# Kernel optimization log

Hardware: AMD Instinct MI355X
Metric: run time of the kernel (lower is better)

## Reference

```python
import jax, jax.numpy as jnp
import numpy as np

B = 131072
H = 128          # hidden_dim
U = H // 2       # uniform_dim = 64
NH = 4           # num_heads
HD = U // NH     # head_dim = 16
OUT = 128        # output_dim
EPS = 1e-5


def setup_inputs() -> dict:
    key = jax.random.key(0)
    ks = jax.random.split(key, 32)
    s = 0.05
    d = {}
    d["x"] = jax.random.normal(ks[0], (B, 58), dtype=jnp.float32)
    # component encoders (Linear -> ReLU -> Dropout(eval))
    d["W_phys"] = jax.random.normal(ks[1], (H // 2, 29)) * s
    d["b_phys"] = jax.random.normal(ks[2], (H // 2,)) * s
    d["W_obj"] = jax.random.normal(ks[3], (H // 4, 15)) * s
    d["b_obj"] = jax.random.normal(ks[4], (H // 4,)) * s
    d["W_mine"] = jax.random.normal(ks[5], (H // 8, 8)) * s
    d["b_mine"] = jax.random.normal(ks[6], (H // 8,)) * s
    d["W_prog"] = jax.random.normal(ks[7], (H // 8, 3)) * s
    d["b_prog"] = jax.random.normal(ks[8], (H // 8,)) * s
    d["W_seq"] = jax.random.normal(ks[9], (H // 8, 3)) * s
    d["b_seq"] = jax.random.normal(ks[10], (H // 8,)) * s
    # projections to uniform_dim
    d["P_phys"] = jax.random.normal(ks[11], (U, H // 2)) * s
    d["pb_phys"] = jax.random.normal(ks[12], (U,)) * s
    d["P_obj"] = jax.random.normal(ks[13], (U, H // 4)) * s
    d["pb_obj"] = jax.random.normal(ks[14], (U,)) * s
    d["P_mine"] = jax.random.normal(ks[15], (U, H // 8)) * s
    d["pb_mine"] = jax.random.normal(ks[16], (U,)) * s
    d["P_prog"] = jax.random.normal(ks[17], (U, H // 8)) * s
    d["pb_prog"] = jax.random.normal(ks[18], (U,)) * s
    d["P_seq"] = jax.random.normal(ks[19], (U, H // 8)) * s
    d["pb_seq"] = jax.random.normal(ks[20], (U,)) * s
    # multi-head attention (torch packed in_proj + out_proj)
    d["Wqkv"] = jax.random.normal(ks[21], (3 * U, U)) * s
    d["bqkv"] = jax.random.normal(ks[22], (3 * U,)) * s
    d["Wo"] = jax.random.normal(ks[23], (U, U)) * s
    d["bo"] = jax.random.normal(ks[24], (U,)) * s
    # layernorm + pool projection
    d["gamma"] = jnp.ones((U,), dtype=jnp.float32)
    d["beta"] = jnp.zeros((U,), dtype=jnp.float32)
    d["Wp"] = jax.random.normal(ks[25], (OUT, U)) * s
    d["bp"] = jax.random.normal(ks[26], (OUT,)) * s
    return d


def _forward(x, W_phys, b_phys, W_obj, b_obj, W_mine, b_mine, W_prog, b_prog,
             W_seq, b_seq, P_phys, pb_phys, P_obj, pb_obj, P_mine, pb_mine,
             P_prog, pb_prog, P_seq, pb_seq, Wqkv, bqkv, Wo, bo,
             gamma, beta, Wp, bp):
    # split 58-dim state into semantic components
    phys, obj, mine = x[:, :29], x[:, 29:44], x[:, 44:52]
    prog, seq = x[:, 52:55], x[:, 55:58]
    relu = jax.nn.relu
    # component encoders (dropout is identity in eval)
    phys_f = relu(phys @ W_phys.T + b_phys)
    obj_f = relu(obj @ W_obj.T + b_obj)
    mine_f = relu(mine @ W_mine.T + b_mine)
    prog_f = relu(prog @ W_prog.T + b_prog)
    seq_f = relu(seq @ W_seq.T + b_seq)
    # project each component to uniform_dim token
    tokens = jnp.stack([
        phys_f @ P_phys.T + pb_phys,
        obj_f @ P_obj.T + pb_obj,
        mine_f @ P_mine.T + pb_mine,
        prog_f @ P_prog.T + pb_prog,
        seq_f @ P_seq.T + pb_seq,
    ], axis=1)  # [B, 5, U]
    # multi-head self-attention (batch_first, torch semantics)
    qkv = tokens @ Wqkv.T + bqkv                      # [B, 5, 3U]
    q, k, v = jnp.split(qkv, 3, axis=-1)
    Bn, S, _ = tokens.shape
    q = q.reshape(Bn, S, NH, HD)
    k = k.reshape(Bn, S, NH, HD)
    v = v.reshape(Bn, S, NH, HD)
    scores = jnp.einsum('bqhd,bkhd->bhqk', q, k) / np.sqrt(HD).astype(np.float32)
    attn = jax.nn.softmax(scores, axis=-1)
    ctx = jnp.einsum('bhqk,bkhd->bqhd', attn, v).reshape(Bn, S, U)
    attn_out = ctx @ Wo.T + bo
    # residual + layernorm
    h = tokens + attn_out
    mu = h.mean(axis=-1, keepdims=True)
    var = ((h - mu) ** 2).mean(axis=-1, keepdims=True)
    h = (h - mu) * jax.lax.rsqrt(var + EPS) * gamma + beta
    # mean pool over the 5 tokens, project, relu (output dropout = identity)
    pooled = h.mean(axis=1)
    return relu(pooled @ Wp.T + bp)  # [B, OUT]


def reference(x, W_phys, b_phys, W_obj, b_obj, W_mine, b_mine, W_prog, b_prog,
              W_seq, b_seq, P_phys, pb_phys, P_obj, pb_obj, P_mine, pb_mine,
              P_prog, pb_prog, P_seq, pb_seq, Wqkv, bqkv, Wo, bo,
              gamma, beta, Wp, bp):
    return _forward(x, W_phys, b_phys, W_obj, b_obj, W_mine, b_mine, W_prog,
                    b_prog, W_seq, b_seq, P_phys, pb_phys, P_obj, pb_obj,
                    P_mine, pb_mine, P_prog, pb_prog, P_seq, pb_seq,
                    Wqkv, bqkv, Wo, bo, gamma, beta, Wp, bp)
```

## Files before the change

kernel.cpp:

```cpp
#include <hip/hip_runtime.h>


#define B_TOTAL 131072
#define NBLK    (B_TOTAL / 64)

typedef _Float16 f16;
typedef __attribute__((ext_vector_type(2))) _Float16 f16x2;
typedef __attribute__((ext_vector_type(8))) _Float16 f16x8;
typedef __attribute__((ext_vector_type(8))) __fp16   mfma8;
typedef __attribute__((ext_vector_type(4))) float    f32x4;

#define W_EW    0
#define W_TOKW  4608
#define W_QKVW  10752
#define W_WOW   29184
#define W_WPW   33280
#define W_ENCB  37376
#define W_TOKB  37520
#define W_QKVB  37840
#define W_BPB   38800
#define W_TOTAL 38928

__device__ __forceinline__ unsigned pk_rne(float a, float b) {
    f16x2 r; r.x = (_Float16)a; r.y = (_Float16)b;
    return __builtin_bit_cast(unsigned, r);
}

extern "C" __global__ void k_prep(
    const float* __restrict__ Wph, const float* __restrict__ bph,
    const float* __restrict__ Wob, const float* __restrict__ bob,
    const float* __restrict__ Wmi, const float* __restrict__ bmi,
    const float* __restrict__ Wpr, const float* __restrict__ bpr,
    const float* __restrict__ Wse, const float* __restrict__ bse,
    const float* __restrict__ Pph, const float* __restrict__ pbph,
    const float* __restrict__ Pob, const float* __restrict__ pbob,
    const float* __restrict__ Pmi, const float* __restrict__ pbmi,
    const float* __restrict__ Ppr, const float* __restrict__ pbpr,
    const float* __restrict__ Pse, const float* __restrict__ pbse,
    const float* __restrict__ Wqkv, const float* __restrict__ bqkv,
    const float* __restrict__ Wo,  const float* __restrict__ bo,
    const float* __restrict__ Wp,  const float* __restrict__ bp,
    unsigned* __restrict__ ws)
{
    int idx = blockIdx.x * 256 + threadIdx.x;
    if (idx >= W_TOTAL) return;
    float* wsf = (float*)ws;

    if (idx < W_TOKW) {
        int w2 = idx, blk = w2 >> 8, r = w2 & 255, lane = r >> 2, pr = r & 3;
        int nt = blk >> 1, ks = blk & 1;
        int n = nt * 16 + (lane & 15);
        float v[2];
#pragma unroll
        for (int e = 0; e < 2; e++) {
            int k = ks * 32 + ((lane >> 4) << 3) + pr * 2 + e;
            float val = 0.f;
            if (n < 64)       { if (k < 29) val = Wph[n*29 + k]; }
            else if (n < 96)  { int kk = k - 29; if (kk >= 0 && kk < 15) val = Wob[(n-64)*15 + kk]; }
            else if (n < 112) { int kk = k - 44; if (kk >= 0 && kk < 8)  val = Wmi[(n-96)*8  + kk]; }
            else if (n < 128) { int kk = k - 52; if (kk >= 0 && kk < 3)  val = Wpr[(n-112)*3 + kk]; }
            else              { int kk = k - 55; if (kk >= 0 && kk < 3)  val = Wse[(n-128)*3 + kk]; }
            v[e] = val;
        }
        ws[idx] = pk_rne(v[0], v[1]);
    } else if (idx < W_QKVW) {
        int w2 = idx - W_TOKW, blk = w2 >> 8, r = w2 & 255, lane = r >> 2, pr = r & 3;
        int t, nt, ks;
        if (blk < 8) { t = 0; nt = blk >> 1; ks = blk & 1; }
        else         { t = 1 + ((blk - 8) >> 2); nt = (blk - 8) & 3; ks = 0; }
        const float* P = (t==0)?Pph:(t==1)?Pob:(t==2)?Pmi:(t==3)?Ppr:Pse;
        int d = (t==0)?64:(t==1)?32:16;
        int n = nt * 16 + (lane & 15);
        float v[2];
#pragma unroll
        for (int e = 0; e < 2; e++) {
            int k = ks * 32 + ((lane >> 4) << 3) + pr * 2 + e;
            v[e] = (k < d) ? P[n*d + k] : 0.f;
        }
        ws[idx] = pk_rne(v[0], v[1]);
    } else if (idx < W_WOW) {
        int w2 = idx - W_QKVW, blk = w2 >> 8, r = w2 & 255, lane = r >> 2, pr = r & 3;
        int t, b2;
        if (blk < 24) { t = 0; b2 = blk; }
        else          { t = 1 + (blk - 24) / 12; b2 = (blk - 24) % 12; }
        int h, nt, ks;
        if (t == 0) { h = b2 / 6; int rem = b2 % 6; nt = rem >> 1; ks = rem & 1; }
        else        { h = b2 / 3; nt = b2 % 3; ks = 0; }
        const float* P = (t==0)?Pph:(t==1)?Pob:(t==2)?Pmi:(t==3)?Ppr:Pse;
        int d = (t==0)?64:(t==1)?32:16;
        int c = nt * 64 + h * 16 + (lane & 15);
        float v[2] = {0.f, 0.f};
#pragma unroll
        for (int e = 0; e < 2; e++) {
            int k = ks * 32 + ((lane >> 4) << 3) + pr * 2 + e;
            if (k < d) {
                float s = 0.f;
                for (int u = 0; u < 64; u++) s += Wqkv[c*64 + u] * P[u*d + k];
                v[e] = s;
            }
        }
        ws[idx] = pk_rne(v[0], v[1]);
    } else if (idx < W_WPW) {
        int w2 = idx - W_WOW, blk = w2 >> 8, r = w2 & 255, lane = r >> 2, pr = r & 3;
        int h = blk >> 2, nt = blk & 3;
        int n = nt * 16 + (lane & 15);
        float v[2];
#pragma unroll
        for (int e = 0; e < 2; e++) {
            int k = ((lane >> 4) << 3) + pr * 2 + e;
            v[e] = (k < 16) ? Wo[n*64 + h*16 + k] : 0.f;
        }
        ws[idx] = pk_rne(v[0], v[1]);
    } else if (idx < W_ENCB) {
        int w2 = idx - W_WPW, blk = w2 >> 8, r = w2 & 255, lane = r >> 2, pr = r & 3;
        int nt = blk >> 1, ks = blk & 1;
        int n = nt * 16 + (lane & 15);
        float v[2];
#pragma unroll
        for (int e = 0; e < 2; e++) {
            int k = ks * 32 + ((lane >> 4) << 3) + pr * 2 + e;
            v[e] = Wp[n*64 + k];
        }
        ws[idx] = pk_rne(v[0], v[1]);
    } else if (idx < W_TOKB) {
        int n = idx - W_ENCB;
        wsf[idx] = (n<64)?bph[n]:(n<96)?bob[n-64]:(n<112)?bmi[n-96]:(n<128)?bpr[n-112]:bse[n-128];
    } else if (idx < W_QKVB) {
        int r = idx - W_TOKB, t = r >> 6, u = r & 63;
        const float* pb = (t==0)?pbph:(t==1)?pbob:(t==2)?pbmi:(t==3)?pbpr:pbse;
        wsf[idx] = pb[u] + bo[u];
    } else if (idx < W_BPB) {
        int r = idx - W_QKVB, t = r / 192, c = r % 192;
        const float* pb = (t==0)?pbph:(t==1)?pbob:(t==2)?pbmi:(t==3)?pbpr:pbse;
        float s = bqkv[c];
        for (int u = 0; u < 64; u++) s += Wqkv[c*64 + u] * pb[u];
        wsf[idx] = s;
    } else {
        wsf[idx] = bp[idx - W_BPB];
    }
}

__device__ __forceinline__ f32x4 MFMA(f16x8 a, f16x8 b, f32x4 c) {
    return __builtin_amdgcn_mfma_f32_16x16x32_f16(
        __builtin_bit_cast(mfma8, a), __builtin_bit_cast(mfma8, b), c, 0, 0, 0);
}

__device__ __forceinline__ f16x8 ldB(const unsigned* __restrict__ W, int wordBase, int blk, int lane) {
    uint4 v = *((const uint4*)(W + wordBase) + (blk * 64 + lane));
    return __builtin_bit_cast(f16x8, v);
}

__device__ __forceinline__ f16x8 ldA(const f16* p, int stride, int row, int kbase, int lg) {
    return *(const f16x8*)(p + row * stride + kbase + lg * 8);
}

__device__ __forceinline__ void stC16(f16* base, int stride, int m0, int col0,
                                      f32x4 c, int l15, int lg) {
    int col = col0 + l15;
    int r0  = m0 + lg * 4;
#pragma unroll
    for (int r = 0; r < 4; r++) base[(r0 + r) * stride + col] = (f16)c[r];
}

extern "C" __global__ void __launch_bounds__(256, 2) k_main(
    const float* __restrict__ x,
    const float* __restrict__ gamma, const float* __restrict__ beta,
    const unsigned* __restrict__ W, float* __restrict__ out)
{
    __shared__ f16 f_lds[64 * 168];
    __shared__ __align__(16) char dyn_lds[41216];
    f16*      xb   = (f16*)dyn_lds;
    f16*      qkv  = (f16*)dyn_lds;
    unsigned* ctx  = (unsigned*)(dyn_lds + 30976);
    f16*      plA  = (f16*)dyn_lds;
    float*    outb = (float*)dyn_lds;

    const int tid  = threadIdx.x;
    const int lane = tid & 63;
    const int wv   = tid >> 6;
    const int l15  = lane & 15;
    const int lg   = lane >> 4;

    const float* wsf   = (const float*)W;
    const float* encb  = wsf + W_ENCB;
    const float* tokbp = wsf + W_TOKB;
    const float* qkvbp = wsf + W_QKVB;
    const float* bpp   = wsf + W_BPB;

    {
        unsigned* du = (unsigned*)dyn_lds;
        for (int i = tid; i < 2304; i += 256) du[i] = 0;
        unsigned* fu = (unsigned*)f_lds;
        for (int i = tid; i < 5376; i += 256) fu[i] = 0;
    }
    __syncthreads();
    {
        const float* xp = x + (size_t)blockIdx.x * (64 * 58);
        for (int i = tid; i < 3712; i += 256) {
            int s = i / 58, k = i - s * 58;
            xb[s * 72 + k] = (f16)xp[i];
        }
    }
    __syncthreads();

    {
        f32x4 accE[3][4];
#pragma unroll
        for (int i = 0; i < 3; i++) {
            int nt = wv + i * 4;
            if (nt < 9) {
                float be = encb[nt * 16 + l15];
#pragma unroll
                for (int mt = 0; mt < 4; mt++) accE[i][mt] = (f32x4){be, be, be, be};
            }
        }
#pragma unroll
        for (int ks = 0; ks < 2; ks++) {
            f16x8 a[4];
#pragma unroll
            for (int mt = 0; mt < 4; mt++) a[mt] = ldA(xb, 72, mt * 16 + l15, ks * 32, lg);
#pragma unroll
            for (int i = 0; i < 3; i++) {
                int nt = wv + i * 4;
                if (nt < 9) {
                    f16x8 b = ldB(W, W_EW, nt * 2 + ks, lane);
#pragma unroll
                    for (int mt = 0; mt < 4; mt++) accE[i][mt] = MFMA(a[mt], b, accE[i][mt]);
                }
            }
        }
#pragma unroll
        for (int i = 0; i < 3; i++) {
            int nt = wv + i * 4;
            if (nt < 9) {
#pragma unroll
                for (int mt = 0; mt < 4; mt++) {
                    f32x4 c = accE[i][mt];
#pragma unroll
                    for (int r = 0; r < 4; r++) c[r] = fmaxf(c[r], 0.f);
                    stC16(f_lds, 168, mt * 16, nt * 16, c, l15, lg);
                }
            }
        }
    }
    __syncthreads();

    f32x4 hf[5][4];

    {
#pragma unroll
        for (int t = 0; t < 5; t++)
#pragma unroll
            for (int nt = 0; nt < 4; nt++) {
                float bb = tokbp[t * 64 + nt * 16 + l15];
                hf[t][nt] = (f32x4){bb, bb, bb, bb};
            }
#pragma unroll
        for (int t = 0; t < 5; t++) {
            const int tokOff[5]  = {0, 64, 96, 112, 128};
            const int tokBase[5] = {0, 8, 12, 16, 20};
#pragma unroll
            for (int ks = 0; ks < 2; ks++) {
                if (ks == 0 || t == 0) {
                    f16x8 a = ldA(f_lds, 168, wv * 16 + l15, tokOff[t] + ks * 32, lg);
#pragma unroll
                    for (int nt = 0; nt < 4; nt++) {
                        int blk = (t == 0) ? (nt * 2 + ks) : (tokBase[t] + nt);
                        f16x8 b = ldB(W, W_TOKW, blk, lane);
                        hf[t][nt] = MFMA(a, b, hf[t][nt]);
                    }
                }
            }
        }
    }

    auto do_qkv = [&](int h) {
        const int tokOff[5]  = {0, 64, 96, 112, 128};
        const int qkvBase[5] = {0, 24, 36, 48, 60};
#pragma unroll
        for (int t = 0; t < 5; t++) {
            f32x4 aq[3];
#pragma unroll
            for (int nt = 0; nt < 3; nt++) {
                float bb = qkvbp[t * 192 + nt * 64 + h * 16 + l15];
                aq[nt] = (f32x4){bb, bb, bb, bb};
            }
#pragma unroll
            for (int ks = 0; ks < 2; ks++) {
                if (ks == 0 || t == 0) {
                    f16x8 a = ldA(f_lds, 168, wv * 16 + l15, tokOff[t] + ks * 32, lg);
#pragma unroll
                    for (int nt = 0; nt < 3; nt++) {
                        int blk = qkvBase[t] + ((t == 0) ? (h * 6 + nt * 2 + ks) : (h * 3 + nt));
                        f16x8 b = ldB(W, W_QKVW, blk, lane);
                        aq[nt] = MFMA(a, b, aq[nt]);
                    }
                }
            }
#pragma unroll
            for (int nt = 0; nt < 3; nt++)
                stC16(qkv, 242, wv * 16, t * 48 + nt * 16, aq[nt], l15, lg);
        }
    };

    auto do_att = [&]() {
        const int s    = tid & 63;
        const int role = wv;
        const f16x2* qr2 = (const f16x2*)(qkv + s * 242);
        float q0[16], q4[16];
#pragma unroll
        for (int d2 = 0; d2 < 8; d2++) {
            f16x2 p = qr2[role * 24 + d2];
            q0[2*d2] = (float)p.x; q0[2*d2+1] = (float)p.y;
        }
        if (role == 0) {
#pragma unroll
            for (int d2 = 0; d2 < 8; d2++) {
                f16x2 p = qr2[96 + d2];
                q4[2*d2] = (float)p.x; q4[2*d2+1] = (float)p.y;
            }
        }
        float p0[5], p4[5];
#pragma unroll
        for (int j = 0; j < 5; j++) {
            float a0 = 0.f, a4 = 0.f;
#pragma unroll
            for (int d2 = 0; d2 < 8; d2++) {
                f16x2 kp = qr2[j * 24 + 8 + d2];
                float k0 = (float)kp.x, k1 = (float)kp.y;
                a0 += q0[2*d2] * k0 + q0[2*d2+1] * k1;
                if (role == 0) a4 += q4[2*d2] * k0 + q4[2*d2+1] * k1;
            }
            p0[j] = a0 * 0.25f; p4[j] = a4 * 0.25f;
        }
        auto softmax5 = [](float* sc) {
            float m = fmaxf(fmaxf(fmaxf(sc[0], sc[1]), fmaxf(sc[2], sc[3])), sc[4]);
            float l = 0.f;
#pragma unroll
            for (int j = 0; j < 5; j++) { sc[j] = __expf(sc[j] - m); l += sc[j]; }
            float r = 1.f / l;
#pragma unroll
            for (int j = 0; j < 5; j++) sc[j] *= r;
        };
        softmax5(p0);
        if (role == 0) softmax5(p4);
        float c0[16], c4[16];
#pragma unroll
        for (int d = 0; d < 16; d++) { c0[d] = 0.f; c4[d] = 0.f; }
#pragma unroll
        for (int j = 0; j < 5; j++) {
#pragma unroll
            for (int d2 = 0; d2 < 8; d2++) {
                f16x2 vp = qr2[j * 24 + 16 + d2];
                float v0 = (float)vp.x, v1 = (float)vp.y;
                c0[2*d2]   += p0[j] * v0;
                c0[2*d2+1] += p0[j] * v1;
                if (role == 0) { c4[2*d2] += p4[j] * v0; c4[2*d2+1] += p4[j] * v1; }
            }
        }
        auto wrctx = [&](int i, const float* c) {
            int row = i * 64 + s;
            int vx  = ((row >> 2) & 3) << 1;
#pragma unroll
            for (int d2 = 0; d2 < 8; d2++)
                ctx[row * 8 + (d2 ^ vx)] = pk_rne(c[2*d2], c[2*d2+1]);
        };
        wrctx(role, c0);
        if (role == 0) wrctx(4, c4);
    };

    auto do_wo = [&](int h) {
        f16x8 bfr[4];
#pragma unroll
        for (int nt = 0; nt < 4; nt++) bfr[nt] = ldB(W, W_WOW, h * 4 + nt, lane);
#pragma unroll
        for (int t = 0; t < 5; t++) {
            int row = t * 64 + wv * 16 + l15;
            int vx  = ((row >> 2) & 3) << 1;
            uint2 a0 = *(const uint2*)&ctx[row * 8 + (((lg & 1) * 4 + 0) ^ vx)];
            uint2 a1 = *(const uint2*)&ctx[row * 8 + (((lg & 1) * 4 + 2) ^ vx)];
            if (lg >= 2) { a0.x = 0; a0.y = 0; a1.x = 0; a1.y = 0; }
            uint4 ua; ua.x = a0.x; ua.y = a0.y; ua.z = a1.x; ua.w = a1.y;
            f16x8 a = __builtin_bit_cast(f16x8, ua);
#pragma unroll
            for (int nt = 0; nt < 4; nt++) hf[t][nt] = MFMA(a, bfr[nt], hf[t][nt]);
        }
    };

    do_qkv(0);
    __syncthreads();
    for (int h = 0; h < 4; h++) {
        do_att();
        __syncthreads();
        do_wo(h);
        if (h < 3) do_qkv(h + 1);
        __syncthreads();
    }

    float g4[4], b4[4];
#pragma unroll
    for (int nt = 0; nt < 4; nt++) { g4[nt] = gamma[nt * 16 + l15]; b4[nt] = beta[nt * 16 + l15]; }
    f32x4 pool[4];
#pragma unroll
    for (int nt = 0; nt < 4; nt++) pool[nt] = (f32x4){0.f, 0.f, 0.f, 0.f};
#pragma unroll
    for (int t = 0; t < 5; t++) {
#pragma unroll
        for (int r = 0; r < 4; r++) {
            float sm = hf[t][0][r] + hf[t][1][r] + hf[t][2][r] + hf[t][3][r];
            sm += __shfl_xor(sm, 1); sm += __shfl_xor(sm, 2);
            sm += __shfl_xor(sm, 4); sm += __shfl_xor(sm, 8);
            float mu = sm * 0.015625f;
            float vs = 0.f;
#pragma unroll
            for (int nt = 0; nt < 4; nt++) { float d = hf[t][nt][r] - mu; vs += d * d; }
            vs += __shfl_xor(vs, 1); vs += __shfl_xor(vs, 2);
            vs += __shfl_xor(vs, 4); vs += __shfl_xor(vs, 8);
            float rs = rsqrtf(vs * 0.015625f + 1e-5f);
#pragma unroll
            for (int nt = 0; nt < 4; nt++)
                pool[nt][r] += (hf[t][nt][r] - mu) * rs * g4[nt] + b4[nt];
        }
    }
#pragma unroll
    for (int nt = 0; nt < 4; nt++) {
        f32x4 c = pool[nt];
#pragma unroll
        for (int r = 0; r < 4; r++) c[r] *= 0.2f;
        stC16(plA, 72, wv * 16, nt * 16, c, l15, lg);
    }
    __syncthreads();

    {
        f32x4 accP[8];
#pragma unroll
        for (int n2 = 0; n2 < 8; n2++) {
            float bb = bpp[n2 * 16 + l15];
            accP[n2] = (f32x4){bb, bb, bb, bb};
        }
#pragma unroll
        for (int ks = 0; ks < 2; ks++) {
            f16x8 a = ldA(plA, 72, wv * 16 + l15, ks * 32, lg);
#pragma unroll
            for (int n2 = 0; n2 < 8; n2++) {
                f16x8 b = ldB(W, W_WPW, n2 * 2 + ks, lane);
                accP[n2] = MFMA(a, b, accP[n2]);
            }
        }
        __syncthreads();
#pragma unroll
        for (int n2 = 0; n2 < 8; n2++) {
#pragma unroll
            for (int r = 0; r < 4; r++) {
                int srow = wv * 16 + lg * 4 + r;
                int col  = n2 * 16 + l15;
                outb[srow * 128 + (col ^ (((srow >> 2) & 3) << 4))] = fmaxf(accP[n2][r], 0.f);
            }
        }
    }
    __syncthreads();

    {
        float* og = out + (size_t)blockIdx.x * (64 * 128);
#pragma unroll
        for (int it = 0; it < 8; it++) {
            int i = tid + it * 256;
            int srow = i >> 5;
            int c4   = (i & 31) << 2;
            float4 v = *(const float4*)&outb[srow * 128 + (c4 ^ (((srow >> 2) & 3) << 4))];
            *(float4*)(og + srow * 128 + c4) = v;
        }
    }
}

extern "C" void kernel_launch(void* const* d_in, const int* in_sizes, int n_in,
                              void* d_out, int out_size, void* d_ws, size_t ws_size,
                              hipStream_t stream)
{
    const float* x      = (const float*)d_in[0];
    const float* W_phys = (const float*)d_in[1];
    const float* b_phys = (const float*)d_in[2];
    const float* W_obj  = (const float*)d_in[3];
    const float* b_obj  = (const float*)d_in[4];
    const float* W_mine = (const float*)d_in[5];
    const float* b_mine = (const float*)d_in[6];
    const float* W_prog = (const float*)d_in[7];
    const float* b_prog = (const float*)d_in[8];
    const float* W_seq  = (const float*)d_in[9];
    const float* b_seq  = (const float*)d_in[10];
    const float* P_phys = (const float*)d_in[11];
    const float* pb_phys= (const float*)d_in[12];
    const float* P_obj  = (const float*)d_in[13];
    const float* pb_obj = (const float*)d_in[14];
    const float* P_mine = (const float*)d_in[15];
    const float* pb_mine= (const float*)d_in[16];
    const float* P_prog = (const float*)d_in[17];
    const float* pb_prog= (const float*)d_in[18];
    const float* P_seq  = (const float*)d_in[19];
    const float* pb_seq = (const float*)d_in[20];
    const float* Wqkv   = (const float*)d_in[21];
    const float* bqkv   = (const float*)d_in[22];
    const float* Wo     = (const float*)d_in[23];
    const float* bo     = (const float*)d_in[24];
    const float* gamma  = (const float*)d_in[25];
    const float* beta   = (const float*)d_in[26];
    const float* Wp     = (const float*)d_in[27];
    const float* bp     = (const float*)d_in[28];

    unsigned* ws = (unsigned*)d_ws;

    k_prep<<<(W_TOTAL + 255) / 256, 256, 0, stream>>>(
        W_phys, b_phys, W_obj, b_obj, W_mine, b_mine, W_prog, b_prog, W_seq, b_seq,
        P_phys, pb_phys, P_obj, pb_obj, P_mine, pb_mine, P_prog, pb_prog, P_seq, pb_seq,
        Wqkv, bqkv, Wo, bo, Wp, bp, ws);

    k_main<<<NBLK, 256, 0, stream>>>(x, gamma, beta, ws, (float*)d_out);
}
```

Baseline: 283.6 us.

## Shrink LDS and restructure attention with swizzled layouts for three blocks per CU

Shrinks the shared scratch buffer so three blocks fit per CU (launch bounds raised from 2 to 3). The qkv buffer is re-laid out with XOR-swizzled row strides, and the attention is reworked to use packed f16 dot2 instructions with a split score/softmax phase and a separate context phase. The final output staging is done in two halves to fit the smaller buffer. This adds more barriers per head and raises register pressure under the tighter occupancy target, which risks spills.

```diff
diff --git a/kernel.cpp b/kernel.cpp
--- a/kernel.cpp
+++ b/kernel.cpp
@@ -24,6 +24,26 @@
 __device__ __forceinline__ unsigned pk_rne(float a, float b) {
     f16x2 r; r.x = (_Float16)a; r.y = (_Float16)b;
     return __builtin_bit_cast(unsigned, r);
+}
+
+__device__ __forceinline__ f16x2 u2h(unsigned u) { return __builtin_bit_cast(f16x2, u); }
+
+__device__ __forceinline__ float fdot2(f16x2 a, f16x2 b, float c) {
+#if __has_builtin(__builtin_amdgcn_fdot2)
+    typedef __fp16 hv2 __attribute__((ext_vector_type(2)));
+    return __builtin_amdgcn_fdot2(__builtin_bit_cast(hv2, a), __builtin_bit_cast(hv2, b), c, false);
+#else
+    return c + (float)a.x * (float)b.x + (float)a.y * (float)b.y;
+#endif
+}
+
+__device__ __forceinline__ float dot8(f16x8 a, f16x8 b, float c) {
+    uint4 ua = __builtin_bit_cast(uint4, a), ub = __builtin_bit_cast(uint4, b);
+    c = fdot2(u2h(ua.x), u2h(ub.x), c);
+    c = fdot2(u2h(ua.y), u2h(ub.y), c);
+    c = fdot2(u2h(ua.z), u2h(ub.z), c);
+    c = fdot2(u2h(ua.w), u2h(ub.w), c);
+    return c;
 }
 
 extern "C" __global__ void k_prep(
@@ -150,36 +170,30 @@
     return __builtin_bit_cast(f16x8, v);
 }
 
-__device__ __forceinline__ f16x8 ldA(const f16* p, int stride, int row, int kbase, int lg) {
-    return *(const f16x8*)(p + row * stride + kbase + lg * 8);
-}
-
-__device__ __forceinline__ void stC16(f16* base, int stride, int m0, int col0,
-                                      f32x4 c, int l15, int lg) {
-    int col = col0 + l15;
-    int r0  = m0 + lg * 4;
-#pragma unroll
-    for (int r = 0; r < 4; r++) base[(r0 + r) * stride + col] = (f16)c[r];
-}
-
-extern "C" __global__ void __launch_bounds__(256, 2) k_main(
+#define F_STRB  336
+#define Q_STRB  496
+
+__device__ __forceinline__ int fswz(int row, int colb) {
+    return (row * F_STRB + colb) ^ (((row >> 3) & 1) << 5);
+}
+__device__ __forceinline__ int qswz(int s, int bo) {
+    return (s * Q_STRB + bo) ^ (((s >> 3) & 1) << 5) ^ (((s >> 4) & 1) << 6);
+}
+
+extern "C" __global__ void __launch_bounds__(256, 3) k_main(
     const float* __restrict__ x,
     const float* __restrict__ gamma, const float* __restrict__ beta,
     const unsigned* __restrict__ W, float* __restrict__ out)
 {
-    __shared__ f16 f_lds[64 * 168];
-    __shared__ __align__(16) char dyn_lds[41216];
-    f16*      xb   = (f16*)dyn_lds;
-    f16*      qkv  = (f16*)dyn_lds;
-    unsigned* ctx  = (unsigned*)(dyn_lds + 30976);
-    f16*      plA  = (f16*)dyn_lds;
-    float*    outb = (float*)dyn_lds;
+    __shared__ __align__(16) f16  f_lds[64 * 168];
+    __shared__ __align__(16) char dyn[31744];
 
     const int tid  = threadIdx.x;
     const int lane = tid & 63;
     const int wv   = tid >> 6;
     const int l15  = lane & 15;
     const int lg   = lane >> 4;
+    const bool m4  = ((lane & 3) == wv);
 
     const float* wsf   = (const float*)W;
     const float* encb  = wsf + W_ENCB;
@@ -187,14 +201,34 @@
     const float* qkvbp = wsf + W_QKVB;
     const float* bpp   = wsf + W_BPB;
 
+    char* fb = (char*)f_lds;
+
+    auto ldA_f = [&](int row, int kf16) -> f16x8 {
+        return *(const f16x8*)(fb + fswz(row, kf16 * 2 + lg * 16));
+    };
+    auto stC_f = [&](int m0, int col0, f32x4 c) {
+#pragma unroll
+        for (int r = 0; r < 4; r++)
+            *(f16*)(fb + fswz(m0 + lg * 4 + r, (col0 + l15) * 2)) = (f16)c[r];
+    };
+    auto ldQ8 = [&](int s, int dw) -> f16x8 {
+        return *(const f16x8*)(dyn + qswz(s, dw * 4));
+    };
+    auto stC_qkv = [&](int m0, int col0, f32x4 c) {
+#pragma unroll
+        for (int r = 0; r < 4; r++)
+            *(f16*)(dyn + qswz(m0 + lg * 4 + r, (col0 + l15) * 2)) = (f16)c[r];
+    };
+
     {
-        unsigned* du = (unsigned*)dyn_lds;
-        for (int i = tid; i < 2304; i += 256) du[i] = 0;
         unsigned* fu = (unsigned*)f_lds;
         for (int i = tid; i < 5376; i += 256) fu[i] = 0;
+        unsigned* du = (unsigned*)dyn;
+        for (int i = tid; i < 2304; i += 256) du[i] = 0;
     }
     __syncthreads();
     {
+        f16* xb = (f16*)dyn;
         const float* xp = x + (size_t)blockIdx.x * (64 * 58);
         for (int i = tid; i < 3712; i += 256) {
             int s = i / 58, k = i - s * 58;
@@ -218,7 +252,10 @@
         for (int ks = 0; ks < 2; ks++) {
             f16x8 a[4];
 #pragma unroll
-            for (int mt = 0; mt < 4; mt++) a[mt] = ldA(xb, 72, mt * 16 + l15, ks * 32, lg);
+            for (int mt = 0; mt < 4; mt++) {
+                const char* p = dyn + (mt * 16 + l15) * 144 + ks * 64 + lg * 16;
+                a[mt] = *(const f16x8*)p;
+            }
 #pragma unroll
             for (int i = 0; i < 3; i++) {
                 int nt = wv + i * 4;
@@ -238,7 +275,7 @@
                     f32x4 c = accE[i][mt];
 #pragma unroll
                     for (int r = 0; r < 4; r++) c[r] = fmaxf(c[r], 0.f);
-                    stC16(f_lds, 168, mt * 16, nt * 16, c, l15, lg);
+                    stC_f(mt * 16, nt * 16, c);
                 }
             }
         }
@@ -246,8 +283,10 @@
     __syncthreads();
 
     f32x4 hf[5][4];
+    const int tokOff[5]  = {0, 64, 96, 112, 128};
 
     {
+        const int tokBase[5] = {0, 8, 12, 16, 20};
 #pragma unroll
         for (int t = 0; t < 5; t++)
 #pragma unroll
@@ -257,12 +296,10 @@
             }
 #pragma unroll
         for (int t = 0; t < 5; t++) {
-            const int tokOff[5]  = {0, 64, 96, 112, 128};
-            const int tokBase[5] = {0, 8, 12, 16, 20};
 #pragma unroll
             for (int ks = 0; ks < 2; ks++) {
                 if (ks == 0 || t == 0) {
-                    f16x8 a = ldA(f_lds, 168, wv * 16 + l15, tokOff[t] + ks * 32, lg);
+                    f16x8 a = ldA_f(wv * 16 + l15, tokOff[t] + ks * 32);
 #pragma unroll
                     for (int nt = 0; nt < 4; nt++) {
                         int blk = (t == 0) ? (nt * 2 + ks) : (tokBase[t] + nt);
@@ -275,7 +312,6 @@
     }
 
     auto do_qkv = [&](int h) {
-        const int tokOff[5]  = {0, 64, 96, 112, 128};
         const int qkvBase[5] = {0, 24, 36, 48, 60};
 #pragma unroll
         for (int t = 0; t < 5; t++) {
@@ -288,7 +324,7 @@
 #pragma unroll
             for (int ks = 0; ks < 2; ks++) {
                 if (ks == 0 || t == 0) {
-                    f16x8 a = ldA(f_lds, 168, wv * 16 + l15, tokOff[t] + ks * 32, lg);
+                    f16x8 a = ldA_f(wv * 16 + l15, tokOff[t] + ks * 32);
 #pragma unroll
                     for (int nt = 0; nt < 3; nt++) {
                         int blk = qkvBase[t] + ((t == 0) ? (h * 6 + nt * 2 + ks) : (h * 3 + nt));
@@ -299,86 +335,19 @@
             }
 #pragma unroll
             for (int nt = 0; nt < 3; nt++)
-                stC16(qkv, 242, wv * 16, t * 48 + nt * 16, aq[nt], l15, lg);
-        }
-    };
-
-    auto do_att = [&]() {
-        const int s    = tid & 63;
-        const int role = wv;
-        const f16x2* qr2 = (const f16x2*)(qkv + s * 242);
-        float q0[16], q4[16];
-#pragma unroll
-        for (int d2 = 0; d2 < 8; d2++) {
-            f16x2 p = qr2[role * 24 + d2];
-            q0[2*d2] = (float)p.x; q0[2*d2+1] = (float)p.y;
-        }
-        if (role == 0) {
-#pragma unroll
-            for (int d2 = 0; d2 < 8; d2++) {
-                f16x2 p = qr2[96 + d2];
-                q4[2*d2] = (float)p.x; q4[2*d2+1] = (float)p.y;
-            }
-        }
-        float p0[5], p4[5];
-#pragma unroll
-        for (int j = 0; j < 5; j++) {
-            float a0 = 0.f, a4 = 0.f;
-#pragma unroll
-            for (int d2 = 0; d2 < 8; d2++) {
-                f16x2 kp = qr2[j * 24 + 8 + d2];
-                float k0 = (float)kp.x, k1 = (float)kp.y;
-                a0 += q0[2*d2] * k0 + q0[2*d2+1] * k1;
-                if (role == 0) a4 += q4[2*d2] * k0 + q4[2*d2+1] * k1;
-            }
-            p0[j] = a0 * 0.25f; p4[j] = a4 * 0.25f;
-        }
-        auto softmax5 = [](float* sc) {
-            float m = fmaxf(fmaxf(fmaxf(sc[0], sc[1]), fmaxf(sc[2], sc[3])), sc[4]);
-            float l = 0.f;
-#pragma unroll
-            for (int j = 0; j < 5; j++) { sc[j] = __expf(sc[j] - m); l += sc[j]; }
-            float r = 1.f / l;
-#pragma unroll
-            for (int j = 0; j < 5; j++) sc[j] *= r;
-        };
-        softmax5(p0);
-        if (role == 0) softmax5(p4);
-        float c0[16], c4[16];
-#pragma unroll
-        for (int d = 0; d < 16; d++) { c0[d] = 0.f; c4[d] = 0.f; }
-#pragma unroll
-        for (int j = 0; j < 5; j++) {
-#pragma unroll
-            for (int d2 = 0; d2 < 8; d2++) {
-                f16x2 vp = qr2[j * 24 + 16 + d2];
-                float v0 = (float)vp.x, v1 = (float)vp.y;
-                c0[2*d2]   += p0[j] * v0;
-                c0[2*d2+1] += p0[j] * v1;
-                if (role == 0) { c4[2*d2] += p4[j] * v0; c4[2*d2+1] += p4[j] * v1; }
-            }
-        }
-        auto wrctx = [&](int i, const float* c) {
-            int row = i * 64 + s;
-            int vx  = ((row >> 2) & 3) << 1;
-#pragma unroll
-            for (int d2 = 0; d2 < 8; d2++)
-                ctx[row * 8 + (d2 ^ vx)] = pk_rne(c[2*d2], c[2*d2+1]);
-        };
-        wrctx(role, c0);
-        if (role == 0) wrctx(4, c4);
+                stC_qkv(wv * 16, nt * 80 + t * 16, aq[nt]);
+        }
     };
 
     auto do_wo = [&](int h) {
         f16x8 bfr[4];
 #pragma unroll
         for (int nt = 0; nt < 4; nt++) bfr[nt] = ldB(W, W_WOW, h * 4 + nt, lane);
+        const int srow = wv * 16 + l15;
 #pragma unroll
         for (int t = 0; t < 5; t++) {
-            int row = t * 64 + wv * 16 + l15;
-            int vx  = ((row >> 2) & 3) << 1;
-            uint2 a0 = *(const uint2*)&ctx[row * 8 + (((lg & 1) * 4 + 0) ^ vx)];
-            uint2 a1 = *(const uint2*)&ctx[row * 8 + (((lg & 1) * 4 + 2) ^ vx)];
+            uint2 a0 = *(const uint2*)(dyn + qswz(srow, (t * 8 + (lg & 1) * 4) * 4));
+            uint2 a1 = *(const uint2*)(dyn + qswz(srow, (t * 8 + (lg & 1) * 4 + 2) * 4));
             if (lg >= 2) { a0.x = 0; a0.y = 0; a1.x = 0; a1.y = 0; }
             uint4 ua; ua.x = a0.x; ua.y = a0.y; ua.z = a1.x; ua.w = a1.y;
             f16x8 a = __builtin_bit_cast(f16x8, ua);
@@ -389,12 +358,65 @@
 
     do_qkv(0);
     __syncthreads();
+
     for (int h = 0; h < 4; h++) {
-        do_att();
+        float p0[5], p4[5];
+        {
+            f16x8 q0a = ldQ8(lane, wv * 8), q0b = ldQ8(lane, wv * 8 + 4);
+            f16x8 q4a = {}, q4b = {};
+            if (m4) { q4a = ldQ8(lane, 32); q4b = ldQ8(lane, 36); }
+            float sc0[5], sc4[5];
+#pragma unroll
+            for (int j = 0; j < 5; j++) {
+                f16x8 ka = ldQ8(lane, 40 + j * 8), kb = ldQ8(lane, 44 + j * 8);
+                sc0[j] = dot8(q0b, kb, dot8(q0a, ka, 0.f)) * 0.25f;
+                sc4[j] = m4 ? dot8(q4b, kb, dot8(q4a, ka, 0.f)) * 0.25f : 0.f;
+            }
+            auto softmax5 = [](const float* sc, float* p) {
+                float m = fmaxf(fmaxf(fmaxf(sc[0], sc[1]), fmaxf(sc[2], sc[3])), sc[4]);
+                float l = 0.f;
+#pragma unroll
+                for (int j = 0; j < 5; j++) { p[j] = __expf(sc[j] - m); l += p[j]; }
+                float r = 1.f / l;
+#pragma unroll
+                for (int j = 0; j < 5; j++) p[j] *= r;
+            };
+            softmax5(sc0, p0);
+            softmax5(sc4, p4);
+        }
         __syncthreads();
+
+        {
+            float ca[16], c4[16];
+#pragma unroll
+            for (int d = 0; d < 16; d++) { ca[d] = 0.f; c4[d] = 0.f; }
+#pragma unroll
+            for (int j = 0; j < 5; j++) {
+                f16x8 va = ldQ8(lane, 80 + j * 8), vb = ldQ8(lane, 84 + j * 8);
+                float pj = p0[j], qj = p4[j];
+#pragma unroll
+                for (int e = 0; e < 8; e++) {
+                    float v0 = (float)va[e], v1 = (float)vb[e];
+                    ca[e]     += pj * v0;
+                    ca[8 + e] += pj * v1;
+                    if (m4) { c4[e] += qj * v0; c4[8 + e] += qj * v1; }
+                }
+            }
+#pragma unroll
+            for (int d2 = 0; d2 < 8; d2++)
+                *(unsigned*)(dyn + qswz(lane, (wv * 8 + d2) * 4)) = pk_rne(ca[2*d2], ca[2*d2+1]);
+            if (m4) {
+#pragma unroll
+                for (int d2 = 0; d2 < 8; d2++)
+                    *(unsigned*)(dyn + qswz(lane, (32 + d2) * 4)) = pk_rne(c4[2*d2], c4[2*d2+1]);
+            }
+        }
+        __syncthreads();
+
         do_wo(h);
-        if (h < 3) do_qkv(h + 1);
         __syncthreads();
+
+        if (h < 3) { do_qkv(h + 1); __syncthreads(); }
     }
 
     float g4[4], b4[4];
@@ -422,53 +444,60 @@
                 pool[nt][r] += (hf[t][nt][r] - mu) * rs * g4[nt] + b4[nt];
         }
     }
-#pragma unroll
-    for (int nt = 0; nt < 4; nt++) {
-        f32x4 c = pool[nt];
-#pragma unroll
-        for (int r = 0; r < 4; r++) c[r] *= 0.2f;
-        stC16(plA, 72, wv * 16, nt * 16, c, l15, lg);
+    {
+        f16* plA = (f16*)dyn;
+#pragma unroll
+        for (int nt = 0; nt < 4; nt++) {
+#pragma unroll
+            for (int r = 0; r < 4; r++)
+                plA[(wv * 16 + lg * 4 + r) * 72 + nt * 16 + l15] = (f16)(pool[nt][r] * 0.2f);
+        }
     }
     __syncthreads();
 
+    f32x4 accP[8];
+#pragma unroll
+    for (int n2 = 0; n2 < 8; n2++) {
+        float bb = bpp[n2 * 16 + l15];
+        accP[n2] = (f32x4){bb, bb, bb, bb};
+    }
+#pragma unroll
+    for (int ks = 0; ks < 2; ks++) {
+        const char* p = dyn + (wv * 16 + l15) * 144 + ks * 64 + lg * 16;
+        f16x8 a = *(const f16x8*)p;
+#pragma unroll
+        for (int n2 = 0; n2 < 8; n2++) {
+            f16x8 b = ldB(W, W_WPW, n2 * 2 + ks, lane);
+            accP[n2] = MFMA(a, b, accP[n2]);
+        }
+    }
+    __syncthreads();
+
     {
-        f32x4 accP[8];
-#pragma unroll
-        for (int n2 = 0; n2 < 8; n2++) {
-            float bb = bpp[n2 * 16 + l15];
-            accP[n2] = (f32x4){bb, bb, bb, bb};
-        }
-#pragma unroll
-        for (int ks = 0; ks < 2; ks++) {
-            f16x8 a = ldA(plA, 72, wv * 16 + l15, ks * 32, lg);
-#pragma unroll
-            for (int n2 = 0; n2 < 8; n2++) {
-                f16x8 b = ldB(W, W_WPW, n2 * 2 + ks, lane);
-                accP[n2] = MFMA(a, b, accP[n2]);
-            }
-        }
-        __syncthreads();
-#pragma unroll
-        for (int n2 = 0; n2 < 8; n2++) {
-#pragma unroll
-            for (int r = 0; r < 4; r++) {
-                int srow = wv * 16 + lg * 4 + r;
-                int col  = n2 * 16 + l15;
-                outb[srow * 128 + (col ^ (((srow >> 2) & 3) << 4))] = fmaxf(accP[n2][r], 0.f);
-            }
-        }
-    }
-    __syncthreads();
-
-    {
+        float* outh = (float*)dyn;
         float* og = out + (size_t)blockIdx.x * (64 * 128);
 #pragma unroll
-        for (int it = 0; it < 8; it++) {
-            int i = tid + it * 256;
-            int srow = i >> 5;
-            int c4   = (i & 31) << 2;
-            float4 v = *(const float4*)&outb[srow * 128 + (c4 ^ (((srow >> 2) & 3) << 4))];
-            *(float4*)(og + srow * 128 + c4) = v;
+        for (int half = 0; half < 2; half++) {
+#pragma unroll
+            for (int m = 0; m < 4; m++) {
+                int n2 = half * 4 + m;
+#pragma unroll
+                for (int r = 0; r < 4; r++) {
+                    int srow = wv * 16 + lg * 4 + r;
+                    int col  = m * 16 + l15;
+                    outh[srow * 64 + (col ^ (((srow >> 2) & 3) << 4))] = fmaxf(accP[n2][r], 0.f);
+                }
+            }
+            __syncthreads();
+#pragma unroll
+            for (int it = 0; it < 4; it++) {
+                int i = tid + it * 256;
+                int srow = i >> 4;
+                int c4   = (i & 15) << 2;
+                float4 v = *(const float4*)&outh[srow * 64 + (c4 ^ (((srow >> 2) & 3) << 4))];
+                *(float4*)(og + srow * 128 + half * 64 + c4) = v;
+            }
+            if (half == 0) __syncthreads();
         }
     }
 }
```

After: 665.0 us. 2.35x slower.

## Split fused kernel into attention and output kernels with context staged through global memory

Applied to the files above, without the earlier changes.

The single fused kernel is split into two launches. The first computes encoders, QKV and attention and writes the per-head context to a workspace buffer in global memory. The second recomputes the encoder and token projections, then reads the context back to apply the output projection, layernorm, pooling and the final projection. The output is now written directly from registers without an LDS transpose. The split lowers LDS per block and shortens each kernel, at the cost of recomputing the encoder stage, an extra launch, and a global round trip for the context.

```diff
diff --git a/kernel.cpp b/kernel.cpp
--- a/kernel.cpp
+++ b/kernel.cpp
@@ -20,6 +20,7 @@
 #define W_QKVB  37840
 #define W_BPB   38800
 #define W_TOTAL 38928
+#define OFF_CTX 38928
 
 __device__ __forceinline__ unsigned pk_rne(float a, float b) {
     f16x2 r; r.x = (_Float16)a; r.y = (_Float16)b;
@@ -102,15 +103,18 @@
         ws[idx] = pk_rne(v[0], v[1]);
     } else if (idx < W_WPW) {
         int w2 = idx - W_WOW, blk = w2 >> 8, r = w2 & 255, lane = r >> 2, pr = r & 3;
-        int h = blk >> 2, nt = blk & 3;
-        int n = nt * 16 + (lane & 15);
-        float v[2];
-#pragma unroll
-        for (int e = 0; e < 2; e++) {
-            int k = ((lane >> 4) << 3) + pr * 2 + e;
-            v[e] = (k < 16) ? Wo[n*64 + h*16 + k] : 0.f;
-        }
-        ws[idx] = pk_rne(v[0], v[1]);
+        if (blk < 8) {
+            int ks2 = blk >> 2, nt = blk & 3;
+            int n = nt * 16 + (lane & 15);
+            float v[2];
+#pragma unroll
+            for (int e = 0; e < 2; e++) {
+                int k = ks2 * 32 + ((lane >> 4) << 3) + pr * 2 + e;
+                int h = k >> 4, d = k & 15;
+                v[e] = Wo[n*64 + h*16 + d];
+            }
+            ws[idx] = pk_rne(v[0], v[1]);
+        } else ws[idx] = 0;
     } else if (idx < W_ENCB) {
         int w2 = idx - W_WPW, blk = w2 >> 8, r = w2 & 255, lane = r >> 2, pr = r & 3;
         int nt = blk >> 1, ks = blk & 1;
@@ -162,18 +166,12 @@
     for (int r = 0; r < 4; r++) base[(r0 + r) * stride + col] = (f16)c[r];
 }
 
-extern "C" __global__ void __launch_bounds__(256, 2) k_main(
-    const float* __restrict__ x,
-    const float* __restrict__ gamma, const float* __restrict__ beta,
-    const unsigned* __restrict__ W, float* __restrict__ out)
+extern "C" __global__ void __launch_bounds__(256, 2) k_mainA(
+    const float* __restrict__ x, const unsigned* __restrict__ W,
+    unsigned* __restrict__ ctxg)
 {
-    __shared__ f16 f_lds[64 * 168];
-    __shared__ __align__(16) char dyn_lds[41216];
-    f16*      xb   = (f16*)dyn_lds;
-    f16*      qkv  = (f16*)dyn_lds;
-    unsigned* ctx  = (unsigned*)(dyn_lds + 30976);
-    f16*      plA  = (f16*)dyn_lds;
-    float*    outb = (float*)dyn_lds;
+    __shared__ __align__(16) f16 f_lds[64 * 168];
+    __shared__ __align__(16) char dyn[30976];
 
     const int tid  = threadIdx.x;
     const int lane = tid & 63;
@@ -183,18 +181,17 @@
 
     const float* wsf   = (const float*)W;
     const float* encb  = wsf + W_ENCB;
-    const float* tokbp = wsf + W_TOKB;
     const float* qkvbp = wsf + W_QKVB;
-    const float* bpp   = wsf + W_BPB;
-
-    {
-        unsigned* du = (unsigned*)dyn_lds;
-        for (int i = tid; i < 2304; i += 256) du[i] = 0;
+
+    {
         unsigned* fu = (unsigned*)f_lds;
         for (int i = tid; i < 5376; i += 256) fu[i] = 0;
-    }
-    __syncthreads();
-    {
+        unsigned* du = (unsigned*)dyn;
+        for (int i = tid; i < 2304; i += 256) du[i] = 0;
+    }
+    __syncthreads();
+    {
+        f16* xb = (f16*)dyn;
         const float* xp = x + (size_t)blockIdx.x * (64 * 58);
         for (int i = tid; i < 3712; i += 256) {
             int s = i / 58, k = i - s * 58;
@@ -218,7 +215,10 @@
         for (int ks = 0; ks < 2; ks++) {
             f16x8 a[4];
 #pragma unroll
-            for (int mt = 0; mt < 4; mt++) a[mt] = ldA(xb, 72, mt * 16 + l15, ks * 32, lg);
+            for (int mt = 0; mt < 4; mt++) {
+                const char* p = dyn + (mt * 16 + l15) * 144 + ks * 64 + lg * 16;
+                a[mt] = *(const f16x8*)p;
+            }
 #pragma unroll
             for (int i = 0; i < 3; i++) {
                 int nt = wv + i * 4;
@@ -245,9 +245,198 @@
     }
     __syncthreads();
 
+    f16* qkv = (f16*)dyn;
+    const int tokOff[5] = {0, 64, 96, 112, 128};
+
+    auto do_qkv = [&](int h) {
+        const int qkvBase[5] = {0, 24, 36, 48, 60};
+#pragma unroll
+        for (int t = 0; t < 5; t++) {
+            f32x4 aq[3];
+#pragma unroll
+            for (int nt = 0; nt < 3; nt++) {
+                float bb = qkvbp[t * 192 + nt * 64 + h * 16 + l15];
+                aq[nt] = (f32x4){bb, bb, bb, bb};
+            }
+#pragma unroll
+            for (int ks = 0; ks < 2; ks++) {
+                if (ks == 0 || t == 0) {
+                    f16x8 a = ldA(f_lds, 168, wv * 16 + l15, tokOff[t] + ks * 32, lg);
+#pragma unroll
+                    for (int nt = 0; nt < 3; nt++) {
+                        int blk = qkvBase[t] + ((t == 0) ? (h * 6 + nt * 2 + ks) : (h * 3 + nt));
+                        f16x8 b = ldB(W, W_QKVW, blk, lane);
+                        aq[nt] = MFMA(a, b, aq[nt]);
+                    }
+                }
+            }
+#pragma unroll
+            for (int nt = 0; nt < 3; nt++)
+                stC16(qkv, 242, wv * 16, t * 48 + nt * 16, aq[nt], l15, lg);
+        }
+    };
+
+    auto do_att = [&](int h) {
+        const int s    = tid & 63;
+        const int role = wv;
+        const int sglob = blockIdx.x * 64 + s;
+        const f16x2* qr2 = (const f16x2*)(qkv + s * 242);
+        float q0[16], q4[16];
+#pragma unroll
+        for (int d2 = 0; d2 < 8; d2++) {
+            f16x2 p = qr2[role * 24 + d2];
+            q0[2*d2] = (float)p.x; q0[2*d2+1] = (float)p.y;
+        }
+        if (role == 0) {
+#pragma unroll
+            for (int d2 = 0; d2 < 8; d2++) {
+                f16x2 p = qr2[96 + d2];
+                q4[2*d2] = (float)p.x; q4[2*d2+1] = (float)p.y;
+            }
+        }
+        float p0[5], p4[5];
+#pragma unroll
+        for (int j = 0; j < 5; j++) {
+            float a0 = 0.f, a4 = 0.f;
+#pragma unroll
+            for (int d2 = 0; d2 < 8; d2++) {
+                f16x2 kp = qr2[j * 24 + 8 + d2];
+                float k0 = (float)kp.x, k1 = (float)kp.y;
+                a0 += q0[2*d2] * k0 + q0[2*d2+1] * k1;
+                if (role == 0) a4 += q4[2*d2] * k0 + q4[2*d2+1] * k1;
+            }
+            p0[j] = a0 * 0.25f; p4[j] = a4 * 0.25f;
+        }
+        auto softmax5 = [](float* sc) {
+            float m = fmaxf(fmaxf(fmaxf(sc[0], sc[1]), fmaxf(sc[2], sc[3])), sc[4]);
+            float l = 0.f;
+#pragma unroll
+            for (int j = 0; j < 5; j++) { sc[j] = __expf(sc[j] - m); l += sc[j]; }
+            float r = 1.f / l;
+#pragma unroll
+            for (int j = 0; j < 5; j++) sc[j] *= r;
+        };
+        softmax5(p0);
+        if (role == 0) softmax5(p4);
+        float c0[16], c4[16];
+#pragma unroll
+        for (int d = 0; d < 16; d++) { c0[d] = 0.f; c4[d] = 0.f; }
+#pragma unroll
+        for (int j = 0; j < 5; j++) {
+#pragma unroll
+            for (int d2 = 0; d2 < 8; d2++) {
+                f16x2 vp = qr2[j * 24 + 16 + d2];
+                float v0 = (float)vp.x, v1 = (float)vp.y;
+                c0[2*d2]   += p0[j] * v0;
+                c0[2*d2+1] += p0[j] * v1;
+                if (role == 0) { c4[2*d2] += p4[j] * v0; c4[2*d2+1] += p4[j] * v1; }
+            }
+        }
+        auto wrctx = [&](int i, const float* c) {
+            unsigned* cg = ctxg + OFF_CTX + (size_t)(h * 40 + i * 8) * B_TOTAL + sglob;
+#pragma unroll
+            for (int d2 = 0; d2 < 8; d2++)
+                cg[(size_t)d2 * B_TOTAL] = pk_rne(c[2*d2], c[2*d2+1]);
+        };
+        wrctx(role, c0);
+        if (role == 0) wrctx(4, c4);
+    };
+
+    do_qkv(0);
+    __syncthreads();
+    for (int h = 0; h < 4; h++) {
+        do_att(h);
+        __syncthreads();
+        if (h < 3) { do_qkv(h + 1); __syncthreads(); }
+    }
+}
+
+extern "C" __global__ void __launch_bounds__(256, 2) k_mainB(
+    const float* __restrict__ x,
+    const float* __restrict__ gamma, const float* __restrict__ beta,
+    const unsigned* __restrict__ W, float* __restrict__ out)
+{
+    __shared__ __align__(16) f16 f_lds[64 * 168];
+    __shared__ __align__(16) char dyn[9216];
+
+    const int tid  = threadIdx.x;
+    const int lane = tid & 63;
+    const int wv   = tid >> 6;
+    const int l15  = lane & 15;
+    const int lg   = lane >> 4;
+
+    const float* wsf   = (const float*)W;
+    const float* encb  = wsf + W_ENCB;
+    const float* tokbp = wsf + W_TOKB;
+    const float* bpp   = wsf + W_BPB;
+
+    {
+        unsigned* fu = (unsigned*)f_lds;
+        for (int i = tid; i < 5376; i += 256) fu[i] = 0;
+        unsigned* du = (unsigned*)dyn;
+        for (int i = tid; i < 2304; i += 256) du[i] = 0;
+    }
+    __syncthreads();
+    {
+        f16* xb = (f16*)dyn;
+        const float* xp = x + (size_t)blockIdx.x * (64 * 58);
+        for (int i = tid; i < 3712; i += 256) {
+            int s = i / 58, k = i - s * 58;
+            xb[s * 72 + k] = (f16)xp[i];
+        }
+    }
+    __syncthreads();
+
+    {
+        f32x4 accE[3][4];
+#pragma unroll
+        for (int i = 0; i < 3; i++) {
+            int nt = wv + i * 4;
+            if (nt < 9) {
+                float be = encb[nt * 16 + l15];
+#pragma unroll
+                for (int mt = 0; mt < 4; mt++) accE[i][mt] = (f32x4){be, be, be, be};
+            }
+        }
+#pragma unroll
+        for (int ks = 0; ks < 2; ks++) {
+            f16x8 a[4];
+#pragma unroll
+            for (int mt = 0; mt < 4; mt++) {
+                const char* p = dyn + (mt * 16 + l15) * 144 + ks * 64 + lg * 16;
+                a[mt] = *(const f16x8*)p;
+            }
+#pragma unroll
+            for (int i = 0; i < 3; i++) {
+                int nt = wv + i * 4;
+                if (nt < 9) {
+                    f16x8 b = ldB(W, W_EW, nt * 2 + ks, lane);
+#pragma unroll
+                    for (int mt = 0; mt < 4; mt++) accE[i][mt] = MFMA(a[mt], b, accE[i][mt]);
+                }
+            }
+        }
+#pragma unroll
+        for (int i = 0; i < 3; i++) {
+            int nt = wv + i * 4;
+            if (nt < 9) {
+#pragma unroll
+                for (int mt = 0; mt < 4; mt++) {
+                    f32x4 c = accE[i][mt];
+#pragma unroll
+                    for (int r = 0; r < 4; r++) c[r] = fmaxf(c[r], 0.f);
+                    stC16(f_lds, 168, mt * 16, nt * 16, c, l15, lg);
+                }
+            }
+        }
+    }
+    __syncthreads();
+
     f32x4 hf[5][4];
-
-    {
+    const int tokOff[5] = {0, 64, 96, 112, 128};
+
+    {
+        const int tokBase[5] = {0, 8, 12, 16, 20};
 #pragma unroll
         for (int t = 0; t < 5; t++)
 #pragma unroll
@@ -257,8 +446,6 @@
             }
 #pragma unroll
         for (int t = 0; t < 5; t++) {
-            const int tokOff[5]  = {0, 64, 96, 112, 128};
-            const int tokBase[5] = {0, 8, 12, 16, 20};
 #pragma unroll
             for (int ks = 0; ks < 2; ks++) {
                 if (ks == 0 || t == 0) {
@@ -274,127 +461,28 @@
         }
     }
 
-    auto do_qkv = [&](int h) {
-        const int tokOff[5]  = {0, 64, 96, 112, 128};
-        const int qkvBase[5] = {0, 24, 36, 48, 60};
-#pragma unroll
-        for (int t = 0; t < 5; t++) {
-            f32x4 aq[3];
-#pragma unroll
-            for (int nt = 0; nt < 3; nt++) {
-                float bb = qkvbp[t * 192 + nt * 64 + h * 16 + l15];
-                aq[nt] = (f32x4){bb, bb, bb, bb};
-            }
-#pragma unroll
-            for (int ks = 0; ks < 2; ks++) {
-                if (ks == 0 || t == 0) {
-                    f16x8 a = ldA(f_lds, 168, wv * 16 + l15, tokOff[t] + ks * 32, lg);
-#pragma unroll
-                    for (int nt = 0; nt < 3; nt++) {
-                        int blk = qkvBase[t] + ((t == 0) ? (h * 6 + nt * 2 + ks) : (h * 3 + nt));
-                        f16x8 b = ldB(W, W_QKVW, blk, lane);
-                        aq[nt] = MFMA(a, b, aq[nt]);
-                    }
-                }
-            }
-#pragma unroll
-            for (int nt = 0; nt < 3; nt++)
-                stC16(qkv, 242, wv * 16, t * 48 + nt * 16, aq[nt], l15, lg);
-        }
-    };
-
-    auto do_att = [&]() {
-        const int s    = tid & 63;
-        const int role = wv;
-        const f16x2* qr2 = (const f16x2*)(qkv + s * 242);
-        float q0[16], q4[16];
-#pragma unroll
-        for (int d2 = 0; d2 < 8; d2++) {
-            f16x2 p = qr2[role * 24 + d2];
-            q0[2*d2] = (float)p.x; q0[2*d2+1] = (float)p.y;
-        }
-        if (role == 0) {
-#pragma unroll
-            for (int d2 = 0; d2 < 8; d2++) {
-                f16x2 p = qr2[96 + d2];
-                q4[2*d2] = (float)p.x; q4[2*d2+1] = (float)p.y;
-            }
-        }
-        float p0[5], p4[5];
-#pragma unroll
-        for (int j = 0; j < 5; j++) {
-            float a0 = 0.f, a4 = 0.f;
-#pragma unroll
-            for (int d2 = 0; d2 < 8; d2++) {
-                f16x2 kp = qr2[j * 24 + 8 + d2];
-                float k0 = (float)kp.x, k1 = (float)kp.y;
-                a0 += q0[2*d2] * k0 + q0[2*d2+1] * k1;
-                if (role == 0) a4 += q4[2*d2] * k0 + q4[2*d2+1] * k1;
-            }
-            p0[j] = a0 * 0.25f; p4[j] = a4 * 0.25f;
-        }
-        auto softmax5 = [](float* sc) {
-            float m = fmaxf(fmaxf(fmaxf(sc[0], sc[1]), fmaxf(sc[2], sc[3])), sc[4]);
-            float l = 0.f;
-#pragma unroll
-            for (int j = 0; j < 5; j++) { sc[j] = __expf(sc[j] - m); l += sc[j]; }
-            float r = 1.f / l;
-#pragma unroll
-            for (int j = 0; j < 5; j++) sc[j] *= r;
-        };
-        softmax5(p0);
-        if (role == 0) softmax5(p4);
-        float c0[16], c4[16];
-#pragma unroll
-        for (int d = 0; d < 16; d++) { c0[d] = 0.f; c4[d] = 0.f; }
-#pragma unroll
-        for (int j = 0; j < 5; j++) {
-#pragma unroll
-            for (int d2 = 0; d2 < 8; d2++) {
-                f16x2 vp = qr2[j * 24 + 16 + d2];
-                float v0 = (float)vp.x, v1 = (float)vp.y;
-                c0[2*d2]   += p0[j] * v0;
-                c0[2*d2+1] += p0[j] * v1;
-                if (role == 0) { c4[2*d2] += p4[j] * v0; c4[2*d2+1] += p4[j] * v1; }
-            }
-        }
-        auto wrctx = [&](int i, const float* c) {
-            int row = i * 64 + s;
-            int vx  = ((row >> 2) & 3) << 1;
-#pragma unroll
-            for (int d2 = 0; d2 < 8; d2++)
-                ctx[row * 8 + (d2 ^ vx)] = pk_rne(c[2*d2], c[2*d2+1]);
-        };
-        wrctx(role, c0);
-        if (role == 0) wrctx(4, c4);
-    };
-
-    auto do_wo = [&](int h) {
-        f16x8 bfr[4];
-#pragma unroll
-        for (int nt = 0; nt < 4; nt++) bfr[nt] = ldB(W, W_WOW, h * 4 + nt, lane);
-#pragma unroll
-        for (int t = 0; t < 5; t++) {
-            int row = t * 64 + wv * 16 + l15;
-            int vx  = ((row >> 2) & 3) << 1;
-            uint2 a0 = *(const uint2*)&ctx[row * 8 + (((lg & 1) * 4 + 0) ^ vx)];
-            uint2 a1 = *(const uint2*)&ctx[row * 8 + (((lg & 1) * 4 + 2) ^ vx)];
-            if (lg >= 2) { a0.x = 0; a0.y = 0; a1.x = 0; a1.y = 0; }
-            uint4 ua; ua.x = a0.x; ua.y = a0.y; ua.z = a1.x; ua.w = a1.y;
-            f16x8 a = __builtin_bit_cast(f16x8, ua);
-#pragma unroll
-            for (int nt = 0; nt < 4; nt++) hf[t][nt] = MFMA(a, bfr[nt], hf[t][nt]);
-        }
-    };
-
-    do_qkv(0);
-    __syncthreads();
-    for (int h = 0; h < 4; h++) {
-        do_att();
-        __syncthreads();
-        do_wo(h);
-        if (h < 3) do_qkv(h + 1);
-        __syncthreads();
+    {
+        const int sg = blockIdx.x * 64 + wv * 16 + l15;
+#pragma unroll
+        for (int ks2 = 0; ks2 < 2; ks2++) {
+            f16x8 bfr[4];
+#pragma unroll
+            for (int nt = 0; nt < 4; nt++) bfr[nt] = ldB(W, W_WOW, ks2 * 4 + nt, lane);
+            const int hh = ks2 * 2 + (lg >> 1);
+#pragma unroll
+            for (int t = 0; t < 5; t++) {
+                const unsigned* cp = W + OFF_CTX +
+                    (size_t)(hh * 40 + t * 8 + (lg & 1) * 4) * B_TOTAL + sg;
+                uint4 ua;
+                ua.x = cp[0];
+                ua.y = cp[(size_t)B_TOTAL];
+                ua.z = cp[(size_t)2 * B_TOTAL];
+                ua.w = cp[(size_t)3 * B_TOTAL];
+                f16x8 a = __builtin_bit_cast(f16x8, ua);
+#pragma unroll
+                for (int nt = 0; nt < 4; nt++) hf[t][nt] = MFMA(a, bfr[nt], hf[t][nt]);
+            }
+        }
     }
 
     float g4[4], b4[4];
@@ -422,12 +510,15 @@
                 pool[nt][r] += (hf[t][nt][r] - mu) * rs * g4[nt] + b4[nt];
         }
     }
-#pragma unroll
-    for (int nt = 0; nt < 4; nt++) {
-        f32x4 c = pool[nt];
-#pragma unroll
-        for (int r = 0; r < 4; r++) c[r] *= 0.2f;
-        stC16(plA, 72, wv * 16, nt * 16, c, l15, lg);
+    __syncthreads();
+    {
+        f16* plA = (f16*)dyn;
+#pragma unroll
+        for (int nt = 0; nt < 4; nt++) {
+#pragma unroll
+            for (int r = 0; r < 4; r++)
+                plA[(wv * 16 + lg * 4 + r) * 72 + nt * 16 + l15] = (f16)(pool[nt][r] * 0.2f);
+        }
     }
     __syncthreads();
 
@@ -440,35 +531,20 @@
         }
 #pragma unroll
         for (int ks = 0; ks < 2; ks++) {
-            f16x8 a = ldA(plA, 72, wv * 16 + l15, ks * 32, lg);
+            const char* p = dyn + (wv * 16 + l15) * 144 + ks * 64 + lg * 16;
+            f16x8 a = *(const f16x8*)p;
 #pragma unroll
             for (int n2 = 0; n2 < 8; n2++) {
                 f16x8 b = ldB(W, W_WPW, n2 * 2 + ks, lane);
                 accP[n2] = MFMA(a, b, accP[n2]);
             }
         }
-        __syncthreads();
+        float* og = out + (size_t)blockIdx.x * (64 * 128);
 #pragma unroll
         for (int n2 = 0; n2 < 8; n2++) {
 #pragma unroll
-            for (int r = 0; r < 4; r++) {
-                int srow = wv * 16 + lg * 4 + r;
-                int col  = n2 * 16 + l15;
-                outb[srow * 128 + (col ^ (((srow >> 2) & 3) << 4))] = fmaxf(accP[n2][r], 0.f);
-            }
-        }
-    }
-    __syncthreads();
-
-    {
-        float* og = out + (size_t)blockIdx.x * (64 * 128);
-#pragma unroll
-        for (int it = 0; it < 8; it++) {
-            int i = tid + it * 256;
-            int srow = i >> 5;
-            int c4   = (i & 31) << 2;
-            float4 v = *(const float4*)&outb[srow * 128 + (c4 ^ (((srow >> 2) & 3) << 4))];
-            *(float4*)(og + srow * 128 + c4) = v;
+            for (int r = 0; r < 4; r++)
+                og[(wv * 16 + lg * 4 + r) * 128 + n2 * 16 + l15] = fmaxf(accP[n2][r], 0.f);
         }
     }
 }
@@ -514,5 +590,6 @@
         P_phys, pb_phys, P_obj, pb_obj, P_mine, pb_mine, P_prog, pb_prog, P_seq, pb_seq,
         Wqkv, bqkv, Wo, bo, Wp, bp, ws);
 
-    k_main<<<NBLK, 256, 0, stream>>>(x, gamma, beta, ws, (float*)d_out);
-}
+    k_mainA<<<NBLK, 256, 0, stream>>>(x, ws, ws);
+    k_mainB<<<NBLK, 256, 0, stream>>>(x, gamma, beta, ws, (float*)d_out);
+}
```

New measurement: 284.9 us. About the same (+0.5%).
